# Performance work log

Hardware: AMD Instinct MI355X
Metric: run time of the kernel (lower is better)

## Reference

```python
import jax, jax.numpy as jnp
import numpy as np

N = 50000          # nodes
E = 800000         # random edges (self-loops appended inside reference)
IN = 32            # input feature dim
HID = 128          # hidden dim (heads * per-head channels)
HEADS = 4
CH = HID // HEADS  # 32 per-head channels
OUT = 6
SLOPE = 0.2        # GATv2 leaky_relu negative slope (PyG default)
EPS = 1e-5


def setup_inputs() -> dict:
    key = jax.random.key(0)
    ks = jax.random.split(key, 24)
    def rn(k, shape, scale=0.05):
        return jax.random.normal(k, shape, dtype=jnp.float32) * scale
    return {
        "x": jax.random.normal(ks[0], (N, IN), dtype=jnp.float32),
        "edge_index": jax.random.randint(ks[1], (2, E), 0, N, dtype=jnp.int32),
        # GATv2 layer 1 (separate source/target transforms, share_weights=False)
        "Wl1": rn(ks[2], (IN, HID)), "Wr1": rn(ks[3], (IN, HID)),
        "att1": rn(ks[4], (HEADS, CH)), "bias1": jnp.zeros((HID,), jnp.float32),
        "g1": jnp.ones((HID,), jnp.float32), "b1": jnp.zeros((HID,), jnp.float32),
        # GATv2 layer 2
        "Wl2": rn(ks[5], (HID, HID)), "Wr2": rn(ks[6], (HID, HID)),
        "att2": rn(ks[7], (HEADS, CH)), "bias2": jnp.zeros((HID,), jnp.float32),
        "g2": jnp.ones((HID,), jnp.float32), "b2": jnp.zeros((HID,), jnp.float32),
        # prediction head: Linear(HID, HID//2) -> ReLU -> Linear(HID//2, OUT)
        "Wp1": rn(ks[8], (HID, HID // 2)), "bp1": jnp.zeros((HID // 2,), jnp.float32),
        "Wp2": rn(ks[9], (HID // 2, OUT)), "bp2": jnp.zeros((OUT,), jnp.float32),
        # uncertainty head: Linear(HID, HID//4) -> ReLU -> Linear(HID//4, OUT) -> Softplus
        "Wu1": rn(ks[10], (HID, HID // 4)), "bu1": jnp.zeros((HID // 4,), jnp.float32),
        "Wu2": rn(ks[11], (HID // 4, OUT)), "bu2": jnp.zeros((OUT,), jnp.float32),
    }


def _gatv2(x, src, dst, Wl, Wr, att, bias):
    # GATv2: e_ij = att . leaky_relu(Wl x_j + Wr x_i); softmax over incoming edges of i
    n = x.shape[0]
    xl = (x @ Wl).reshape(n, HEADS, CH)   # source (message) transform
    xr = (x @ Wr).reshape(n, HEADS, CH)   # target transform
    el = xl[src]                           # [E, H, C] gather
    e = jax.nn.leaky_relu(el + xr[dst], SLOPE)
    s = jnp.einsum('ehc,hc->eh', e, att)   # [E, H] attention logits
    m = jax.ops.segment_max(s, dst, num_segments=n)          # stable softmax per dst
    a = jnp.exp(s - m[dst])
    denom = jax.ops.segment_sum(a, dst, num_segments=n)
    alpha = a / denom[dst]                 # [E, H]
    out = jax.ops.segment_sum(el * alpha[:, :, None], dst, num_segments=n)
    return out.reshape(n, HID) + bias


def _ln(h, g, b):
    mu = jnp.mean(h, axis=-1, keepdims=True)
    v = jnp.var(h, axis=-1, keepdims=True)
    return (h - mu) * jax.lax.rsqrt(v + EPS) * g + b


def reference(x, edge_index, Wl1, Wr1, att1, bias1, g1, b1,
              Wl2, Wr2, att2, bias2, g2, b2,
              Wp1, bp1, Wp2, bp2, Wu1, bu1, Wu2, bu2):
    n = x.shape[0]
    loops = jnp.arange(n, dtype=edge_index.dtype)
    ei = jnp.concatenate([edge_index, jnp.stack([loops, loops])], axis=1)
    src, dst = ei[0], ei[1]
    h = _gatv2(x, src, dst, Wl1, Wr1, att1, bias1)
    h = jax.nn.elu(_ln(h, g1, b1))
    h2 = _gatv2(h, src, dst, Wl2, Wr2, att2, bias2)
    h2 = _ln(h2, g2, b2)
    h = jax.nn.elu(h + h2)
    pred = jnp.maximum(h @ Wp1 + bp1, 0.0) @ Wp2 + bp2
    uncertainty = jax.nn.softplus(jnp.maximum(h @ Wu1 + bu1, 0.0) @ Wu2 + bu2)
    return pred, uncertainty
```

## Files before the change

### kernel.cpp

```cpp
#include <hip/hip_runtime.h>
#include <hip/hip_bf16.h>
#include <math.h>

#define HID 128
#define HEADS 4
#define CH 32
#define OUTD 6
#define SLOPE 0.2f
#define LNEPS 1e-5f

static inline int cdiv(int a, int b) { return (a + b - 1) / b; }

__device__ __forceinline__ float bf2f(unsigned short u) {
    unsigned int v = ((unsigned int)u) << 16;
    return __builtin_bit_cast(float, v);
}
__device__ __forceinline__ unsigned short f2bf(float f) {
    unsigned int u = __builtin_bit_cast(unsigned int, f);
    u += 0x7FFFu + ((u >> 16) & 1u);
    return (unsigned short)(u >> 16);
}
__device__ __forceinline__ float bflo(unsigned int u) {
    return __builtin_bit_cast(float, u << 16);
}
__device__ __forceinline__ float bfhi(unsigned int u) {
    return __builtin_bit_cast(float, u & 0xFFFF0000u);
}


__global__ void k_count_rank(const int* __restrict__ ei, int E, int n,
                             int* __restrict__ deg, int* __restrict__ epos) {
    int e = blockIdx.x * 256 + threadIdx.x;
    int EA = E + n;
    if (e >= EA) return;
    int dst = (e < E) ? ei[E + e] : (e - E);
    epos[e] = atomicAdd(&deg[dst], 1);
}

__global__ __launch_bounds__(1024) void k_scan1(const int* __restrict__ deg, int n,
                                                int* __restrict__ ex, int* __restrict__ bsum) {
    __shared__ int sw[16];
    int i = blockIdx.x * 1024 + threadIdx.x;
    int v = (i < n) ? deg[i] : 0;
    int lane = threadIdx.x & 63, w = threadIdx.x >> 6;
    int x = v;
    #pragma unroll
    for (int d = 1; d < 64; d <<= 1) {
        int t = __shfl_up(x, d);
        if (lane >= d) x += t;
    }
    if (lane == 63) sw[w] = x;
    __syncthreads();
    if (w == 0) {
        int t = (lane < 16) ? sw[lane] : 0;
        #pragma unroll
        for (int d = 1; d < 16; d <<= 1) {
            int u = __shfl_up(t, d);
            if (lane >= d) t += u;
        }
        if (lane < 16) sw[lane] = t;
    }
    __syncthreads();
    int woff = (w > 0) ? sw[w - 1] : 0;
    int incl = x + woff;
    if (i < n) ex[i] = incl - v;
    if (threadIdx.x == 1023) bsum[blockIdx.x] = incl;
}

__global__ void k_scan2(int* __restrict__ bsum, int nb) {
    int lane = threadIdx.x;
    int v = (lane < nb) ? bsum[lane] : 0;
    int x = v;
    #pragma unroll
    for (int d = 1; d < 64; d <<= 1) {
        int t = __shfl_up(x, d);
        if (lane >= d) x += t;
    }
    if (lane < nb) bsum[lane] = x - v;
}

__global__ __launch_bounds__(1024) void k_scan3(int* __restrict__ ex, const int* __restrict__ bsum, int n) {
    int i = blockIdx.x * 1024 + threadIdx.x;
    if (i < n) ex[i] += bsum[blockIdx.x];
}

__global__ void k_scatter(const int* __restrict__ ei, const int* __restrict__ epos,
                          const int* __restrict__ offsets, int E, int n,
                          int* __restrict__ csr_src) {
    int e = blockIdx.x * 256 + threadIdx.x;
    int EA = E + n;
    if (e >= EA) return;
    int src, dst;
    if (e < E) { src = ei[e]; dst = ei[E + e]; }
    else       { src = dst = e - E; }
    csr_src[offsets[dst] + epos[e]] = src;
}

template <int K>
__global__ __launch_bounds__(256) void dual_linear(const float* __restrict__ X,
                                                   const float* __restrict__ Wl,
                                                   const float* __restrict__ Wr,
                                                   unsigned short* __restrict__ outL,
                                                   float* __restrict__ outR, int n) {
    __shared__ float sX[32][K + 4];
    int tid = threadIdx.x;
    int tx = tid & 63;
    int ty = tid >> 6;
    int node0 = blockIdx.x * 32;

    constexpr int C4 = K / 4;
    constexpr int NQ = (32 * C4) / 256;
    #pragma unroll
    for (int q = 0; q < NQ; ++q) {
        int g = q * 256 + tid;
        int row = g / C4, c4 = g % C4;
        int gn = node0 + row;
        float4 v = make_float4(0.f, 0.f, 0.f, 0.f);
        if (gn < n) v = *(const float4*)&X[(size_t)gn * K + c4 * 4];
        *(float4*)&sX[row][c4 * 4] = v;
    }
    __syncthreads();

    const float* Wbase = (tx < 32) ? (Wl + tx * 4) : (Wr + (tx - 32) * 4);

    float4 acc[8];
    #pragma unroll
    for (int i = 0; i < 8; ++i) acc[i] = make_float4(0.f, 0.f, 0.f, 0.f);

    #pragma unroll 2
    for (int k4 = 0; k4 < K / 4; ++k4) {
        const float* wp = Wbase + (size_t)k4 * 4 * HID;
        float4 w0 = *(const float4*)(wp);
        float4 w1 = *(const float4*)(wp + HID);
        float4 w2 = *(const float4*)(wp + 2 * HID);
        float4 w3 = *(const float4*)(wp + 3 * HID);
        #pragma unroll
        for (int i = 0; i < 8; ++i) {
            float4 xq = *(const float4*)&sX[ty * 8 + i][k4 * 4];
            acc[i].x = fmaf(xq.x, w0.x, acc[i].x);
            acc[i].y = fmaf(xq.x, w0.y, acc[i].y);
            acc[i].z = fmaf(xq.x, w0.z, acc[i].z);
            acc[i].w = fmaf(xq.x, w0.w, acc[i].w);
            acc[i].x = fmaf(xq.y, w1.x, acc[i].x);
            acc[i].y = fmaf(xq.y, w1.y, acc[i].y);
            acc[i].z = fmaf(xq.y, w1.z, acc[i].z);
            acc[i].w = fmaf(xq.y, w1.w, acc[i].w);
            acc[i].x = fmaf(xq.z, w2.x, acc[i].x);
            acc[i].y = fmaf(xq.z, w2.y, acc[i].y);
            acc[i].z = fmaf(xq.z, w2.z, acc[i].z);
            acc[i].w = fmaf(xq.z, w2.w, acc[i].w);
            acc[i].x = fmaf(xq.w, w3.x, acc[i].x);
            acc[i].y = fmaf(xq.w, w3.y, acc[i].y);
            acc[i].z = fmaf(xq.w, w3.z, acc[i].z);
            acc[i].w = fmaf(xq.w, w3.w, acc[i].w);
        }
    }

    int c = tx * 4;
    if (c < HID) {
        #pragma unroll
        for (int i = 0; i < 8; ++i) {
            int gn = node0 + ty * 8 + i;
            if (gn < n) {
                ushort4 o;
                o.x = f2bf(acc[i].x); o.y = f2bf(acc[i].y);
                o.z = f2bf(acc[i].z); o.w = f2bf(acc[i].w);
                *(ushort4*)&outL[(size_t)gn * HID + c] = o;
            }
        }
    } else {
        int cc = c - HID;
        #pragma unroll
        for (int i = 0; i < 8; ++i) {
            int gn = node0 + ty * 8 + i;
            if (gn < n) *(float4*)&outR[(size_t)gn * HID + cc] = acc[i];
        }
    }
}


struct GatAcc {
    float den;
    float nb[8];
};

__device__ __forceinline__ void gat_edge(uint4 r, bool valid,
                                         const float4& xrA, const float4& xrB,
                                         const float4& atA, const float4& atB,
                                         GatAcc& g) {
    float e0 = bflo(r.x), e1 = bfhi(r.x);
    float e2 = bflo(r.y), e3 = bfhi(r.y);
    float e4 = bflo(r.z), e5 = bfhi(r.z);
    float e6 = bflo(r.w), e7 = bfhi(r.w);
    float v0 = e0 + xrA.x; v0 = fmaxf(v0, SLOPE * v0);
    float v1 = e1 + xrA.y; v1 = fmaxf(v1, SLOPE * v1);
    float v2 = e2 + xrA.z; v2 = fmaxf(v2, SLOPE * v2);
    float v3 = e3 + xrA.w; v3 = fmaxf(v3, SLOPE * v3);
    float v4 = e4 + xrB.x; v4 = fmaxf(v4, SLOPE * v4);
    float v5 = e5 + xrB.y; v5 = fmaxf(v5, SLOPE * v5);
    float v6 = e6 + xrB.z; v6 = fmaxf(v6, SLOPE * v6);
    float v7 = e7 + xrB.w; v7 = fmaxf(v7, SLOPE * v7);
    float t = v0 * atA.x;
    t = fmaf(v1, atA.y, t);
    t = fmaf(v2, atA.z, t);
    t = fmaf(v3, atA.w, t);
    t = fmaf(v4, atB.x, t);
    t = fmaf(v5, atB.y, t);
    t = fmaf(v6, atB.z, t);
    t = fmaf(v7, atB.w, t);
    t += __shfl_xor(t, 1);
    t += __shfl_xor(t, 2);
    float a = valid ? __expf(t) : 0.f;
    g.den += a;
    g.nb[0] = fmaf(a, e0, g.nb[0]);
    g.nb[1] = fmaf(a, e1, g.nb[1]);
    g.nb[2] = fmaf(a, e2, g.nb[2]);
    g.nb[3] = fmaf(a, e3, g.nb[3]);
    g.nb[4] = fmaf(a, e4, g.nb[4]);
    g.nb[5] = fmaf(a, e5, g.nb[5]);
    g.nb[6] = fmaf(a, e6, g.nb[6]);
    g.nb[7] = fmaf(a, e7, g.nb[7]);
}

__global__ __launch_bounds__(256) void gat_aggr(const unsigned short* __restrict__ xl,
                                                const float* __restrict__ xr,
                                                const int* __restrict__ csr_src,
                                                const int* __restrict__ offsets,
                                                const int* __restrict__ deg,
                                                const float* __restrict__ att,
                                                const float* __restrict__ bias,
                                                const float* __restrict__ gamma,
                                                const float* __restrict__ beta,
                                                const float* __restrict__ hprev,
                                                float* __restrict__ hout,
                                                int n, int layer) {
    int wave = threadIdx.x >> 6;
    int lane = threadIdx.x & 63;
    int dst = blockIdx.x * 4 + wave;
    if (dst >= n) return;

    int lc = lane & 15;
    int eg = lane >> 4;
    int c0 = lc * 8;

    float4 atA = *(const float4*)&att[c0];
    float4 atB = *(const float4*)&att[c0 + 4];
    const float* xrp = &xr[(size_t)dst * HID + c0];
    float4 xrA = *(const float4*)xrp;
    float4 xrB = *(const float4*)(xrp + 4);

    int start = offsets[dst];
    int cnt = deg[dst];
    const int* sp = csr_src + start;

    GatAcc g;
    g.den = 0.f;
    #pragma unroll
    for (int j = 0; j < 8; ++j) g.nb[j] = 0.f;

    for (int base = 0; base < cnt; base += 64) {
        int rem = cnt - base;
        int vidx = (lane < rem) ? sp[base + lane] : 0;
        int qmax = ((rem < 64 ? rem : 64) + 3) >> 2;
        int q = 0;
        for (; q + 2 <= qmax; q += 2) {
            int slot0 = q * 4 + eg;
            int slot1 = slot0 + 4;
            int s0 = __shfl(vidx, slot0);
            int s1 = __shfl(vidx, slot1);
            uint4 r0 = *(const uint4*)(xl + ((size_t)s0 << 7) + c0);
            uint4 r1 = *(const uint4*)(xl + ((size_t)s1 << 7) + c0);
            gat_edge(r0, slot0 < rem, xrA, xrB, atA, atB, g);
            gat_edge(r1, slot1 < rem, xrA, xrB, atA, atB, g);
        }
        for (; q < qmax; ++q) {
            int slot0 = q * 4 + eg;
            int s0 = __shfl(vidx, slot0);
            uint4 r0 = *(const uint4*)(xl + ((size_t)s0 << 7) + c0);
            gat_edge(r0, slot0 < rem, xrA, xrB, atA, atB, g);
        }
    }

    g.den += __shfl_xor(g.den, 16);
    g.den += __shfl_xor(g.den, 32);
    #pragma unroll
    for (int j = 0; j < 8; ++j) {
        g.nb[j] += __shfl_xor(g.nb[j], 16);
        g.nb[j] += __shfl_xor(g.nb[j], 32);
    }

    float inv = 1.f / g.den;
    float4 bA = *(const float4*)&bias[c0];
    float4 bB = *(const float4*)&bias[c0 + 4];
    float v[8];
    v[0] = fmaf(g.nb[0], inv, bA.x);
    v[1] = fmaf(g.nb[1], inv, bA.y);
    v[2] = fmaf(g.nb[2], inv, bA.z);
    v[3] = fmaf(g.nb[3], inv, bA.w);
    v[4] = fmaf(g.nb[4], inv, bB.x);
    v[5] = fmaf(g.nb[5], inv, bB.y);
    v[6] = fmaf(g.nb[6], inv, bB.z);
    v[7] = fmaf(g.nb[7], inv, bB.w);

    float s1 = 0.f, s2 = 0.f;
    #pragma unroll
    for (int j = 0; j < 8; ++j) {
        s1 += v[j];
        s2 = fmaf(v[j], v[j], s2);
    }
    #pragma unroll
    for (int d = 1; d < 16; d <<= 1) {
        s1 += __shfl_xor(s1, d);
        s2 += __shfl_xor(s2, d);
    }
    float mu = s1 * (1.f / 128.f);
    float var = s2 * (1.f / 128.f) - mu * mu;
    float rs = rsqrtf(var + LNEPS);

    float4 gA = *(const float4*)&gamma[c0];
    float4 gB = *(const float4*)&gamma[c0 + 4];
    float4 beA = *(const float4*)&beta[c0];
    float4 beB = *(const float4*)&beta[c0 + 4];
    float y[8];
    y[0] = (v[0] - mu) * rs * gA.x + beA.x;
    y[1] = (v[1] - mu) * rs * gA.y + beA.y;
    y[2] = (v[2] - mu) * rs * gA.z + beA.z;
    y[3] = (v[3] - mu) * rs * gA.w + beA.w;
    y[4] = (v[4] - mu) * rs * gB.x + beB.x;
    y[5] = (v[5] - mu) * rs * gB.y + beB.y;
    y[6] = (v[6] - mu) * rs * gB.z + beB.z;
    y[7] = (v[7] - mu) * rs * gB.w + beB.w;

    if (layer == 2) {
        const float* hp = &hprev[(size_t)dst * HID + c0];
        float4 hA = *(const float4*)hp;
        float4 hB = *(const float4*)(hp + 4);
        y[0] += hA.x; y[1] += hA.y; y[2] += hA.z; y[3] += hA.w;
        y[4] += hB.x; y[5] += hB.y; y[6] += hB.z; y[7] += hB.w;
    }
    #pragma unroll
    for (int j = 0; j < 8; ++j)
        y[j] = (y[j] > 0.f) ? y[j] : (__expf(y[j]) - 1.f);

    if (eg == 0) {
        float* op = &hout[(size_t)dst * HID + c0];
        *(float4*)op = make_float4(y[0], y[1], y[2], y[3]);
        *(float4*)(op + 4) = make_float4(y[4], y[5], y[6], y[7]);
    }
}

__global__ __launch_bounds__(256) void k_heads(const float* __restrict__ hf,
                                               const float* __restrict__ Wp1, const float* __restrict__ bp1,
                                               const float* __restrict__ Wp2, const float* __restrict__ bp2,
                                               const float* __restrict__ Wu1, const float* __restrict__ bu1,
                                               const float* __restrict__ Wu2, const float* __restrict__ bu2,
                                               float* __restrict__ out, int n) {
    __shared__ float sXH[64 * 132];
    __shared__ float sW[32 * 96];
    __shared__ float sW2[64 * 6 + 32 * 6];
    int tid = threadIdx.x;
    int node0 = blockIdx.x * 64;

    for (int i = tid; i < 576; i += 256) sW2[i] = (i < 384) ? Wp2[i] : Wu2[i - 384];

    {
        int row = tid >> 2, seg = tid & 3;
        int gn = node0 + row;
        const float* src = &hf[(size_t)gn * HID + seg * 32];
        float* dst = &sXH[row * 132 + seg * 32];
        #pragma unroll
        for (int q = 0; q < 8; ++q) {
            float4 v = make_float4(0.f, 0.f, 0.f, 0.f);
            if (gn < n) v = *(const float4*)&src[q * 4];
            *(float4*)&dst[q * 4] = v;
        }
    }

    int cg = tid & 15;
    int ng = tid >> 4;
    int c0 = cg * 6;

    float acc[4][6];
    #pragma unroll
    for (int i = 0; i < 4; ++i)
        #pragma unroll
        for (int j = 0; j < 6; ++j) acc[i][j] = 0.f;

    for (int kc = 0; kc < HID; kc += 32) {
        __syncthreads();
        #pragma unroll
        for (int q = 0; q < 3; ++q) {
            int g = q * 256 + tid;
            int r = g / 24, c4 = g % 24;
            int c = c4 * 4;
            const float* src = (c < 64) ? &Wp1[(size_t)(kc + r) * 64 + c]
                                        : &Wu1[(size_t)(kc + r) * 32 + (c - 64)];
            *(float4*)&sW[r * 96 + c] = *(const float4*)src;
        }
        __syncthreads();
        #pragma unroll
        for (int k = 0; k < 32; ++k) {
            const float* wr = &sW[k * 96 + c0];
            float w0 = wr[0], w1 = wr[1], w2 = wr[2], w3 = wr[3], w4 = wr[4], w5 = wr[5];
            #pragma unroll
            for (int i = 0; i < 4; ++i) {
                float xv = sXH[(ng * 4 + i) * 132 + kc + k];
                acc[i][0] = fmaf(xv, w0, acc[i][0]);
                acc[i][1] = fmaf(xv, w1, acc[i][1]);
                acc[i][2] = fmaf(xv, w2, acc[i][2]);
                acc[i][3] = fmaf(xv, w3, acc[i][3]);
                acc[i][4] = fmaf(xv, w4, acc[i][4]);
                acc[i][5] = fmaf(xv, w5, acc[i][5]);
            }
        }
    }

    __syncthreads();
    float bv[6];
    #pragma unroll
    for (int j = 0; j < 6; ++j) {
        int c = c0 + j;
        bv[j] = (c < 64) ? bp1[c] : bu1[c - 64];
    }
    #pragma unroll
    for (int i = 0; i < 4; ++i) {
        int row = ng * 4 + i;
        #pragma unroll
        for (int j = 0; j < 6; ++j) {
            float v = acc[i][j] + bv[j];
            sXH[row * 97 + c0 + j] = fmaxf(v, 0.f);
        }
    }
    __syncthreads();

    int nl = tid & 63;
    int g = tid >> 6;
    int node = node0 + nl;
    float a0 = 0.f, a1 = 0.f, a2 = 0.f;
    if (g < 2) {
        int j0 = 3 * g;
        const float* hrow = &sXH[nl * 97];
        #pragma unroll 8
        for (int k = 0; k < 64; ++k) {
            float hv = hrow[k];
            a0 = fmaf(hv, sW2[k * 6 + j0], a0);
            a1 = fmaf(hv, sW2[k * 6 + j0 + 1], a1);
            a2 = fmaf(hv, sW2[k * 6 + j0 + 2], a2);
        }
        if (node < n) {
            size_t pb = (size_t)node * 6 + j0;
            out[pb]     = a0 + bp2[j0];
            out[pb + 1] = a1 + bp2[j0 + 1];
            out[pb + 2] = a2 + bp2[j0 + 2];
        }
    } else {
        int j0 = 3 * (g - 2);
        const float* hrow = &sXH[nl * 97 + 64];
        #pragma unroll 8
        for (int k = 0; k < 32; ++k) {
            float hv = hrow[k];
            a0 = fmaf(hv, sW2[384 + k * 6 + j0], a0);
            a1 = fmaf(hv, sW2[384 + k * 6 + j0 + 1], a1);
            a2 = fmaf(hv, sW2[384 + k * 6 + j0 + 2], a2);
        }
        if (node < n) {
            float z0 = a0 + bu2[j0], z1 = a1 + bu2[j0 + 1], z2 = a2 + bu2[j0 + 2];
            size_t ub = (size_t)n * 6 + (size_t)node * 6 + j0;
            out[ub]     = fmaxf(z0, 0.f) + log1pf(__expf(-fabsf(z0)));
            out[ub + 1] = fmaxf(z1, 0.f) + log1pf(__expf(-fabsf(z1)));
            out[ub + 2] = fmaxf(z2, 0.f) + log1pf(__expf(-fabsf(z2)));
        }
    }
}


extern "C" void kernel_launch(void* const* d_in, const int* in_sizes, int n_in,
                              void* d_out, int out_size, void* d_ws, size_t ws_size,
                              hipStream_t stream) {
    const float* x   = (const float*)d_in[0];
    const int*   ei  = (const int*)d_in[1];
    const float* Wl1 = (const float*)d_in[2];
    const float* Wr1 = (const float*)d_in[3];
    const float* att1 = (const float*)d_in[4];
    const float* bias1 = (const float*)d_in[5];
    const float* g1 = (const float*)d_in[6];
    const float* b1 = (const float*)d_in[7];
    const float* Wl2 = (const float*)d_in[8];
    const float* Wr2 = (const float*)d_in[9];
    const float* att2 = (const float*)d_in[10];
    const float* bias2 = (const float*)d_in[11];
    const float* g2 = (const float*)d_in[12];
    const float* b2 = (const float*)d_in[13];
    const float* Wp1 = (const float*)d_in[14];
    const float* bp1 = (const float*)d_in[15];
    const float* Wp2 = (const float*)d_in[16];
    const float* bp2 = (const float*)d_in[17];
    const float* Wu1 = (const float*)d_in[18];
    const float* bu1 = (const float*)d_in[19];
    const float* Wu2 = (const float*)d_in[20];
    const float* bu2 = (const float*)d_in[21];

    int N_ = in_sizes[0] / 32;
    int E_ = in_sizes[1] / 2;
    int EA = E_ + N_;

    char* p = (char*)d_ws;
    size_t fbytes = (size_t)N_ * HID * sizeof(float);
    unsigned short* xl = (unsigned short*)p; p += fbytes / 2;
    float* xr = (float*)p; p += fbytes;
    float* h  = (float*)p; p += fbytes;
    float* hf = (float*)p; p += fbytes;
    auto align16 = [](size_t s) { return (s + 15) & ~(size_t)15; };
    int* deg     = (int*)p; p += align16((size_t)N_ * 4);
    int* offsets = (int*)p; p += align16((size_t)N_ * 4);
    int* bsum    = (int*)p; p += 64 * 4;
    int* csr_src = (int*)p; p += align16((size_t)EA * 4);
    int* epos = (int*)hf;

    hipMemsetAsync(deg, 0, (size_t)N_ * 4, stream);

    int nScan = cdiv(N_, 1024);
    k_count_rank<<<cdiv(EA, 256), 256, 0, stream>>>(ei, E_, N_, deg, epos);
    k_scan1<<<nScan, 1024, 0, stream>>>(deg, N_, offsets, bsum);
    k_scan2<<<1, 64, 0, stream>>>(bsum, nScan);
    k_scan3<<<nScan, 1024, 0, stream>>>(offsets, bsum, N_);
    k_scatter<<<cdiv(EA, 256), 256, 0, stream>>>(ei, epos, offsets, E_, N_, csr_src);

    dual_linear<32><<<cdiv(N_, 32), 256, 0, stream>>>(x, Wl1, Wr1, xl, xr, N_);
    gat_aggr<<<cdiv(N_, 4), 256, 0, stream>>>(xl, xr, csr_src, offsets, deg,
                                              att1, bias1, g1, b1, nullptr, h, N_, 1);
    dual_linear<128><<<cdiv(N_, 32), 256, 0, stream>>>(h, Wl2, Wr2, xl, xr, N_);
    gat_aggr<<<cdiv(N_, 4), 256, 0, stream>>>(xl, xr, csr_src, offsets, deg,
                                              att2, bias2, g2, b2, h, hf, N_, 2);
    k_heads<<<cdiv(N_, 64), 256, 0, stream>>>(hf, Wp1, bp1, Wp2, bp2,
                                              Wu1, bu1, Wu2, bu2, (float*)d_out, N_);
}
```

Baseline: 361.0 us.

## Store target transform in bf16, enlarge linear tile, split edge loop tail

The target-side projection xr is now written and read as bf16 instead of fp32, halving its storage and read traffic in the aggregation kernel. The dual linear kernel processes 64 nodes per block with 16 accumulators per thread, doubling the reuse of each weight load. The edge loop splits full groups of four edges from a masked tail, so the validity select is skipped in the common path, and it uses 32-bit byte-offset addressing for the gathers. Risks are slightly lower precision in the attention logits and higher register pressure in the linear kernel.

After: 366.1 us. Within noise of the previous version (+1.4%).

```diff
diff --git a/kernel.cpp b/kernel.cpp
--- a/kernel.cpp
+++ b/kernel.cpp
@@ -11,10 +11,6 @@
 
 static inline int cdiv(int a, int b) { return (a + b - 1) / b; }
 
-__device__ __forceinline__ float bf2f(unsigned short u) {
-    unsigned int v = ((unsigned int)u) << 16;
-    return __builtin_bit_cast(float, v);
-}
 __device__ __forceinline__ unsigned short f2bf(float f) {
     unsigned int u = __builtin_bit_cast(unsigned int, f);
     u += 0x7FFFu + ((u >> 16) & 1u);
@@ -101,15 +97,15 @@
                                                    const float* __restrict__ Wl,
                                                    const float* __restrict__ Wr,
                                                    unsigned short* __restrict__ outL,
-                                                   float* __restrict__ outR, int n) {
-    __shared__ float sX[32][K + 4];
+                                                   unsigned short* __restrict__ outR, int n) {
+    __shared__ float sX[64][K + 4];
     int tid = threadIdx.x;
     int tx = tid & 63;
     int ty = tid >> 6;
-    int node0 = blockIdx.x * 32;
+    int node0 = blockIdx.x * 64;
 
     constexpr int C4 = K / 4;
-    constexpr int NQ = (32 * C4) / 256;
+    constexpr int NQ = (64 * C4) / 256;
     #pragma unroll
     for (int q = 0; q < NQ; ++q) {
         int g = q * 256 + tid;
@@ -123,9 +119,9 @@
 
     const float* Wbase = (tx < 32) ? (Wl + tx * 4) : (Wr + (tx - 32) * 4);
 
-    float4 acc[8];
-    #pragma unroll
-    for (int i = 0; i < 8; ++i) acc[i] = make_float4(0.f, 0.f, 0.f, 0.f);
+    float4 acc[16];
+    #pragma unroll
+    for (int i = 0; i < 16; ++i) acc[i] = make_float4(0.f, 0.f, 0.f, 0.f);
 
     #pragma unroll 2
     for (int k4 = 0; k4 < K / 4; ++k4) {
@@ -135,8 +131,8 @@
         float4 w2 = *(const float4*)(wp + 2 * HID);
         float4 w3 = *(const float4*)(wp + 3 * HID);
         #pragma unroll
-        for (int i = 0; i < 8; ++i) {
-            float4 xq = *(const float4*)&sX[ty * 8 + i][k4 * 4];
+        for (int i = 0; i < 16; ++i) {
+            float4 xq = *(const float4*)&sX[ty * 16 + i][k4 * 4];
             acc[i].x = fmaf(xq.x, w0.x, acc[i].x);
             acc[i].y = fmaf(xq.x, w0.y, acc[i].y);
             acc[i].z = fmaf(xq.x, w0.z, acc[i].z);
@@ -157,23 +153,16 @@
     }
 
     int c = tx * 4;
-    if (c < HID) {
-        #pragma unroll
-        for (int i = 0; i < 8; ++i) {
-            int gn = node0 + ty * 8 + i;
-            if (gn < n) {
-                ushort4 o;
-                o.x = f2bf(acc[i].x); o.y = f2bf(acc[i].y);
-                o.z = f2bf(acc[i].z); o.w = f2bf(acc[i].w);
-                *(ushort4*)&outL[(size_t)gn * HID + c] = o;
-            }
-        }
-    } else {
-        int cc = c - HID;
-        #pragma unroll
-        for (int i = 0; i < 8; ++i) {
-            int gn = node0 + ty * 8 + i;
-            if (gn < n) *(float4*)&outR[(size_t)gn * HID + cc] = acc[i];
+    unsigned short* basep = (c < HID) ? outL : outR;
+    int cc = (c < HID) ? c : c - HID;
+    #pragma unroll
+    for (int i = 0; i < 16; ++i) {
+        int gn = node0 + ty * 16 + i;
+        if (gn < n) {
+            ushort4 o;
+            o.x = f2bf(acc[i].x); o.y = f2bf(acc[i].y);
+            o.z = f2bf(acc[i].z); o.w = f2bf(acc[i].w);
+            *(ushort4*)&basep[(size_t)gn * HID + cc] = o;
         }
     }
 }
@@ -184,6 +173,7 @@
     float nb[8];
 };
 
+template <bool CHECKED>
 __device__ __forceinline__ void gat_edge(uint4 r, bool valid,
                                          const float4& xrA, const float4& xrB,
                                          const float4& atA, const float4& atB,
@@ -210,7 +200,8 @@
     t = fmaf(v7, atB.w, t);
     t += __shfl_xor(t, 1);
     t += __shfl_xor(t, 2);
-    float a = valid ? __expf(t) : 0.f;
+    float a = __expf(t);
+    if (CHECKED) a = valid ? a : 0.f;
     g.den += a;
     g.nb[0] = fmaf(a, e0, g.nb[0]);
     g.nb[1] = fmaf(a, e1, g.nb[1]);
@@ -223,7 +214,7 @@
 }
 
 __global__ __launch_bounds__(256) void gat_aggr(const unsigned short* __restrict__ xl,
-                                                const float* __restrict__ xr,
+                                                const unsigned short* __restrict__ xr,
                                                 const int* __restrict__ csr_src,
                                                 const int* __restrict__ offsets,
                                                 const int* __restrict__ deg,
@@ -242,12 +233,15 @@
     int lc = lane & 15;
     int eg = lane >> 4;
     int c0 = lc * 8;
+    unsigned cb = (unsigned)(lc * 16);
 
     float4 atA = *(const float4*)&att[c0];
     float4 atB = *(const float4*)&att[c0 + 4];
-    const float* xrp = &xr[(size_t)dst * HID + c0];
-    float4 xrA = *(const float4*)xrp;
-    float4 xrB = *(const float4*)(xrp + 4);
+    const char* xlb = (const char*)xl;
+
+    uint4 xrr = *(const uint4*)((const char*)xr + (unsigned)dst * 256u + cb);
+    float4 xrA = make_float4(bflo(xrr.x), bfhi(xrr.x), bflo(xrr.y), bfhi(xrr.y));
+    float4 xrB = make_float4(bflo(xrr.z), bfhi(xrr.z), bflo(xrr.w), bfhi(xrr.w));
 
     int start = offsets[dst];
     int cnt = deg[dst];
@@ -260,24 +254,31 @@
 
     for (int base = 0; base < cnt; base += 64) {
         int rem = cnt - base;
-        int vidx = (lane < rem) ? sp[base + lane] : 0;
-        int qmax = ((rem < 64 ? rem : 64) + 3) >> 2;
+        int lim = rem < 64 ? rem : 64;
+        int vidx = (lane < lim) ? sp[base + lane] : 0;
+        int fq = lim >> 2;
         int q = 0;
-        for (; q + 2 <= qmax; q += 2) {
-            int slot0 = q * 4 + eg;
-            int slot1 = slot0 + 4;
-            int s0 = __shfl(vidx, slot0);
-            int s1 = __shfl(vidx, slot1);
-            uint4 r0 = *(const uint4*)(xl + ((size_t)s0 << 7) + c0);
-            uint4 r1 = *(const uint4*)(xl + ((size_t)s1 << 7) + c0);
-            gat_edge(r0, slot0 < rem, xrA, xrB, atA, atB, g);
-            gat_edge(r1, slot1 < rem, xrA, xrB, atA, atB, g);
-        }
-        for (; q < qmax; ++q) {
+        for (; q + 2 <= fq; q += 2) {
             int slot0 = q * 4 + eg;
             int s0 = __shfl(vidx, slot0);
-            uint4 r0 = *(const uint4*)(xl + ((size_t)s0 << 7) + c0);
-            gat_edge(r0, slot0 < rem, xrA, xrB, atA, atB, g);
+            int s1 = __shfl(vidx, slot0 + 4);
+            uint4 r0 = *(const uint4*)(xlb + (((unsigned)s0 << 8) + cb));
+            uint4 r1 = *(const uint4*)(xlb + (((unsigned)s1 << 8) + cb));
+            gat_edge<false>(r0, true, xrA, xrB, atA, atB, g);
+            gat_edge<false>(r1, true, xrA, xrB, atA, atB, g);
+        }
+        if (q < fq) {
+            int slot0 = q * 4 + eg;
+            int s0 = __shfl(vidx, slot0);
+            uint4 r0 = *(const uint4*)(xlb + (((unsigned)s0 << 8) + cb));
+            gat_edge<false>(r0, true, xrA, xrB, atA, atB, g);
+        }
+        int tail = lim & 3;
+        if (tail) {
+            int slot0 = fq * 4 + eg;
+            int s0 = __shfl(vidx, slot0);
+            uint4 r0 = *(const uint4*)(xlb + (((unsigned)s0 << 8) + cb));
+            gat_edge<true>(r0, eg < tail, xrA, xrB, atA, atB, g);
         }
     }
 
@@ -507,7 +508,7 @@
     char* p = (char*)d_ws;
     size_t fbytes = (size_t)N_ * HID * sizeof(float);
     unsigned short* xl = (unsigned short*)p; p += fbytes / 2;
-    float* xr = (float*)p; p += fbytes;
+    unsigned short* xr = (unsigned short*)p; p += fbytes / 2;
     float* h  = (float*)p; p += fbytes;
     float* hf = (float*)p; p += fbytes;
     auto align16 = [](size_t s) { return (s + 15) & ~(size_t)15; };
@@ -526,10 +527,10 @@
     k_scan3<<<nScan, 1024, 0, stream>>>(offsets, bsum, N_);
     k_scatter<<<cdiv(EA, 256), 256, 0, stream>>>(ei, epos, offsets, E_, N_, csr_src);
 
-    dual_linear<32><<<cdiv(N_, 32), 256, 0, stream>>>(x, Wl1, Wr1, xl, xr, N_);
+    dual_linear<32><<<cdiv(N_, 64), 256, 0, stream>>>(x, Wl1, Wr1, xl, xr, N_);
     gat_aggr<<<cdiv(N_, 4), 256, 0, stream>>>(xl, xr, csr_src, offsets, deg,
                                               att1, bias1, g1, b1, nullptr, h, N_, 1);
-    dual_linear<128><<<cdiv(N_, 32), 256, 0, stream>>>(h, Wl2, Wr2, xl, xr, N_);
+    dual_linear<128><<<cdiv(N_, 64), 256, 0, stream>>>(h, Wl2, Wr2, xl, xr, N_);
     gat_aggr<<<cdiv(N_, 4), 256, 0, stream>>>(xl, xr, csr_src, offsets, deg,
                                               att2, bias2, g2, b2, h, hf, N_, 2);
     k_heads<<<cdiv(N_, 64), 256, 0, stream>>>(hf, Wp1, bp1, Wp2, bp2,
```
